# Optimization experiments

Measured on AMD Instinct MI355X. Metric: run time of the kernel, lower is better.

Reference implementation:

```python
import jax, jax.numpy as jnp
import numpy as np

NSMP = 8192
NA = 512  # min_in_features
DOUT = 256  # out_features
REALNA = 520  # input.shape[1] - nSmp


def setup_inputs() -> dict:
    key = jax.random.key(0)
    k1, k2 = jax.random.split(key)
    inp = jax.random.uniform(k1, (NSMP, REALNA + NSMP), dtype=jnp.float32)
    weight = jax.random.uniform(k2, (NA, DOUT), dtype=jnp.float32)  # torch.rand init
    return {"input": inp, "weight": weight}


def reference(input, weight):
    nSmp = NSMP
    na = NA
    X = input[:, :na]  # [nSmp, na]
    realna = input.shape[1] - nSmp
    A = input[:, realna - 8:realna + nSmp - 8]  # [nSmp, nSmp]
    A = A + jnp.eye(nSmp, dtype=input.dtype)
    # D = diag(colsum(A)); D_hat = inverse(D)**0.5 == diag(d^{-1/2})
    d = jnp.sum(A, axis=0)
    d_inv_sqrt = jax.lax.rsqrt(d)
    # DAD = D_hat @ A @ D_hat, applied as row/col scaling (exploits diagonal structure)
    DAD = d_inv_sqrt[:, None] * A * d_inv_sqrt[None, :]
    support = X @ weight  # [nSmp, out]
    output = DAD @ support  # [nSmp, out]
    # bias=False in init, so no bias add
    return jnp.concatenate((output, A), axis=1)  # [nSmp, out + nSmp]
```

## Files before the change

kernel.cpp:

```cpp
#include <hip/hip_runtime.h>

#define NSMP 8192
#define INW  8712
#define OUTW 8448
#define AOFF 512
#define DO   256

typedef __attribute__((ext_vector_type(4)))  float f32x4;
typedef __attribute__((ext_vector_type(8)))  short short8;
typedef __attribute__((ext_vector_type(16))) float floatx16;

typedef __attribute__((address_space(1))) const unsigned int* gptr_t;
typedef __attribute__((address_space(3)))       unsigned int* lptr_t;

__device__ __forceinline__ unsigned pk_bf16(float lo, float hi) {
    return (__float_as_uint(lo) >> 16) | (__float_as_uint(hi) & 0xffff0000u);
}

__device__ __forceinline__ void gload_lds16(const void* g, void* l) {
    __builtin_amdgcn_global_load_lds((gptr_t)g, (lptr_t)l, 16, 0, 0);
}

__global__ __launch_bounds__(256) void kcopy(const float* __restrict__ in,
                                             float* __restrict__ out,
                                             float* __restrict__ d) {
    const int t  = threadIdx.x;
    const int j0 = blockIdx.x * 1024;
    const int i0 = blockIdx.y * 32;
    const int jc = j0 + 4 * t;
    const float* src = in  + (size_t)i0 * INW  + AOFF + jc;
    float*       dst = out + (size_t)i0 * OUTW + DO   + jc;
    f32x4 cs = {0.f, 0.f, 0.f, 0.f};
#pragma unroll 8
    for (int r = 0; r < 32; ++r) {
        f32x4 v = *(const f32x4*)(src + (size_t)r * INW);
        int di = (i0 + r) - j0;
        if ((di >> 2) == t) {
            int s = di & 3;
            v[0] += (s == 0); v[1] += (s == 1); v[2] += (s == 2); v[3] += (s == 3);
        }
        cs += v;
        __builtin_nontemporal_store(v, (f32x4*)(dst + (size_t)r * OUTW));
    }
    atomicAdd(&d[jc + 0], cs[0]);
    atomicAdd(&d[jc + 1], cs[1]);
    atomicAdd(&d[jc + 2], cs[2]);
    atomicAdd(&d[jc + 3], cs[3]);
}

__global__ __launch_bounds__(256) void ksupport(const float* __restrict__ in,
                                                const float* __restrict__ w,
                                                const float* __restrict__ d,
                                                float* __restrict__ dinv,
                                                unsigned short* __restrict__ sP) {
    const int c  = threadIdx.x;
    const int r0 = blockIdx.x * 8;
    const float* X = in + (size_t)r0 * INW;
    float acc[8] = {0.f, 0.f, 0.f, 0.f, 0.f, 0.f, 0.f, 0.f};
#pragma unroll 4
    for (int k = 0; k < 512; ++k) {
        float wv = w[(size_t)k * DO + c];
#pragma unroll
        for (int r = 0; r < 8; ++r)
            acc[r] = fmaf(X[(size_t)r * INW + k], wv, acc[r]);
    }
    union { unsigned short h[8]; uint4 u; } pk;
#pragma unroll
    for (int r = 0; r < 8; ++r) {
        float dv = rsqrtf(d[r0 + r]);
        unsigned ub = __float_as_uint(acc[r] * dv);
        ub += 0x7fffu + ((ub >> 16) & 1u);
        pk.h[r] = (unsigned short)(ub >> 16);
    }
    *(uint4*)(sP + (size_t)(r0 >> 3) * (DO * 8) + (size_t)c * 8) = pk.u;
    if (c < 8) dinv[r0 + c] = rsqrtf(d[r0 + c]);
}

__global__ __launch_bounds__(256, 2) void kmm(const float* __restrict__ in,
                                              const unsigned short* __restrict__ sP,
                                              const float* __restrict__ dinv,
                                              float* __restrict__ out) {
    __shared__ __align__(16) float          lA[2][32 * 64];
    __shared__ __align__(16) unsigned short lB[2][8 * 128 * 8];

    const int b  = blockIdx.x;
    const int rg = ((b >> 4) << 3) + (b & 7);
    const int ch = (b >> 3) & 1;
    const int tid = threadIdx.x;
    const int w = tid >> 6, lane = tid & 63;
    const int m = lane & 31, q = lane >> 5;
    const int i0 = rg * 32;
    const int cc = ch * 128 + w * 32 + m;

    const int subr = lane >> 4;
    const int gl   = lane & 15;
    const int lrA0 = w * 8;

    floatx16 acc;
#pragma unroll
    for (int z = 0; z < 16; ++z) acc[z] = 0.f;

    auto stage = [&](int nb, int s) {
        const int k0 = s * 64;
#pragma unroll
        for (int t = 0; t < 2; ++t) {
            const int lr = lrA0 + t * 4 + subr;
            const float* g = in + (size_t)(i0 + lr) * INW + AOFF + k0 + 4 * (gl ^ (lr & 7));
            gload_lds16(g, &lA[nb][(lrA0 + t * 4) * 64]);
        }
#pragma unroll
        for (int j = 0; j < 4; ++j) {
            const int oct  = 2 * w + (j >> 1);
            const int ch64 = j & 1;
            const unsigned short* g = sP + (size_t)(s * 8 + oct) * (DO * 8)
                                        + (size_t)(ch * 128 + ch64 * 64 + lane) * 8;
            gload_lds16(g, &lB[nb][(oct * 128 + ch64 * 64) * 8]);
        }
    };

    stage(0, 0);
    __syncthreads();

    for (int s = 0; s < 128; ++s) {
        const int cur = s & 1;
        if (s + 1 < 128) stage(cur ^ 1, s + 1);
        const float*          lAc = lA[cur];
        const unsigned short* lBc = lB[cur];
#pragma unroll
        for (int ks = 0; ks < 4; ++ks) {
            const int gbase = ks * 4 + q * 2;
            const int g0 = gbase ^ (m & 7);
            const int g1 = (gbase + 1) ^ (m & 7);
            f32x4 a0 = *(const f32x4*)(lAc + m * 64 + g0 * 4);
            f32x4 a1 = *(const f32x4*)(lAc + m * 64 + g1 * 4);
            uint4 bq = *(const uint4*)(lBc + ((size_t)(2 * ks + q) * 128 + w * 32 + m) * 8);
            union { unsigned u[4]; short8 s8; } fa;
            fa.u[0] = pk_bf16(a0[0], a0[1]); fa.u[1] = pk_bf16(a0[2], a0[3]);
            fa.u[2] = pk_bf16(a1[0], a1[1]); fa.u[3] = pk_bf16(a1[2], a1[3]);
            union { uint4 q4; short8 s8; } fb; fb.q4 = bq;
            acc = __builtin_amdgcn_mfma_f32_32x32x16_bf16(fa.s8, fb.s8, acc, 0, 0, 0);
        }
        __syncthreads();
    }

#pragma unroll
    for (int g = 0; g < 4; ++g) {
        const ushort4 s4 = *(const ushort4*)(sP + (size_t)(i0 / 8 + g) * (DO * 8)
                                                + (size_t)cc * 8 + 4 * q);
        unsigned short sv[4] = {s4.x, s4.y, s4.z, s4.w};
#pragma unroll
        for (int rr = 0; rr < 4; ++rr) {
            const int row = i0 + 8 * g + 4 * q + rr;
            const float idt = __uint_as_float(((unsigned)sv[rr]) << 16);
            out[(size_t)row * OUTW + cc] = (acc[g * 4 + rr] + idt) * dinv[row];
        }
    }
}

extern "C" void kernel_launch(void* const* d_in, const int* in_sizes, int n_in,
                              void* d_out, int out_size, void* d_ws, size_t ws_size,
                              hipStream_t stream) {
    (void)in_sizes; (void)n_in; (void)out_size; (void)ws_size;
    const float* in = (const float*)d_in[0];
    const float* w  = (const float*)d_in[1];
    float* out  = (float*)d_out;
    float* d    = (float*)d_ws;
    float* dinv = d + NSMP;
    unsigned short* sP = (unsigned short*)(d + 2 * NSMP);

    hipMemsetAsync(d, 0, NSMP * sizeof(float), stream);
    kcopy<<<dim3(8, 256), 256, 0, stream>>>(in, out, d);
    ksupport<<<1024, 256, 0, stream>>>(in, w, d, dinv, sP);
    kmm<<<512, 256, 0, stream>>>(in, sP, dinv, out);
}
```

Measured before the change: 671.4 us.

## Emit bf16 copy of A in copy kernel and stream it in matmul

The copy kernel now also writes a bf16 version of A (without the identity) into workspace, so the matmul kernel reads half the bytes for A and skips the per-iteration fp32-to-bf16 packing. The B operand (scaled support) is now loaded straight into registers instead of through shared memory, and the main loop is unrolled by two with explicit double buffering. This adds an extra 128MB bf16 write in the copy kernel in exchange for reading 128MB instead of 256MB in the matmul. A-loads in the copy kernel are also marked nontemporal.

```diff
diff --git a/kernel.cpp b/kernel.cpp
--- a/kernel.cpp
+++ b/kernel.cpp
@@ -23,17 +23,23 @@
 
 __global__ __launch_bounds__(256) void kcopy(const float* __restrict__ in,
                                              float* __restrict__ out,
-                                             float* __restrict__ d) {
+                                             float* __restrict__ d,
+                                             unsigned short* __restrict__ aP) {
     const int t  = threadIdx.x;
     const int j0 = blockIdx.x * 1024;
     const int i0 = blockIdx.y * 32;
     const int jc = j0 + 4 * t;
-    const float* src = in  + (size_t)i0 * INW  + AOFF + jc;
-    float*       dst = out + (size_t)i0 * OUTW + DO   + jc;
+    const float*    src = in  + (size_t)i0 * INW  + AOFF + jc;
+    float*          dst = out + (size_t)i0 * OUTW + DO   + jc;
+    unsigned short* ap  = aP  + (size_t)i0 * NSMP + jc;
     f32x4 cs = {0.f, 0.f, 0.f, 0.f};
 #pragma unroll 8
     for (int r = 0; r < 32; ++r) {
-        f32x4 v = *(const f32x4*)(src + (size_t)r * INW);
+        f32x4 v = __builtin_nontemporal_load((const f32x4*)(src + (size_t)r * INW));
+        uint2 pb;
+        pb.x = pk_bf16(v[0], v[1]);
+        pb.y = pk_bf16(v[2], v[3]);
+        *(uint2*)(ap + (size_t)r * NSMP) = pb;
         int di = (i0 + r) - j0;
         if ((di >> 2) == t) {
             int s = di & 3;
@@ -76,12 +82,11 @@
     if (c < 8) dinv[r0 + c] = rsqrtf(d[r0 + c]);
 }
 
-__global__ __launch_bounds__(256, 2) void kmm(const float* __restrict__ in,
+__global__ __launch_bounds__(256, 2) void kmm(const unsigned short* __restrict__ aP,
                                               const unsigned short* __restrict__ sP,
                                               const float* __restrict__ dinv,
                                               float* __restrict__ out) {
-    __shared__ __align__(16) float          lA[2][32 * 64];
-    __shared__ __align__(16) unsigned short lB[2][8 * 128 * 8];
+    __shared__ __align__(16) unsigned short lA[2][32 * 64];
 
     const int b  = blockIdx.x;
     const int rg = ((b >> 4) << 3) + (b & 7);
@@ -92,56 +97,56 @@
     const int i0 = rg * 32;
     const int cc = ch * 128 + w * 32 + m;
 
-    const int subr = lane >> 4;
-    const int gl   = lane & 15;
-    const int lrA0 = w * 8;
+    const int srow = lane >> 3;
+    const int sg   = lane & 7;
+    const unsigned short* aSrc = aP + (size_t)(i0 + w * 8 + srow) * NSMP
+                                    + 8 * (sg ^ (srow & 7));
+    const unsigned short* bB   = sP + (size_t)q * 2048 + (size_t)cc * 8;
 
     floatx16 acc;
 #pragma unroll
     for (int z = 0; z < 16; ++z) acc[z] = 0.f;
 
-    auto stage = [&](int nb, int s) {
-        const int k0 = s * 64;
-#pragma unroll
-        for (int t = 0; t < 2; ++t) {
-            const int lr = lrA0 + t * 4 + subr;
-            const float* g = in + (size_t)(i0 + lr) * INW + AOFF + k0 + 4 * (gl ^ (lr & 7));
-            gload_lds16(g, &lA[nb][(lrA0 + t * 4) * 64]);
-        }
-#pragma unroll
-        for (int j = 0; j < 4; ++j) {
-            const int oct  = 2 * w + (j >> 1);
-            const int ch64 = j & 1;
-            const unsigned short* g = sP + (size_t)(s * 8 + oct) * (DO * 8)
-                                        + (size_t)(ch * 128 + ch64 * 64 + lane) * 8;
-            gload_lds16(g, &lB[nb][(oct * 128 + ch64 * 64) * 8]);
-        }
-    };
+    uint4 Ba0, Ba1, Ba2, Ba3, Bb0, Bb1, Bb2, Bb3;
 
-    stage(0, 0);
+#define STAGE_A(nb, s) gload_lds16(aSrc + (size_t)(s) * 64, &lA[nb][w * 512])
+#define LOAD_B(P, s) do {                                              \
+        P##0 = *(const uint4*)(bB + (size_t)((s) * 8 + 0) * 2048);     \
+        P##1 = *(const uint4*)(bB + (size_t)((s) * 8 + 2) * 2048);     \
+        P##2 = *(const uint4*)(bB + (size_t)((s) * 8 + 4) * 2048);     \
+        P##3 = *(const uint4*)(bB + (size_t)((s) * 8 + 6) * 2048);     \
+    } while (0)
+#define MFMA_KS(cur, Breg, ks) do {                                    \
+        union { uint4 u; short8 s8; } fb_; fb_.u = Breg;               \
+        const short8 af_ = *(const short8*)(                           \
+            &lA[cur][m * 64 + ((((ks) * 2 + q) ^ (m & 7)) * 8)]);      \
+        acc = __builtin_amdgcn_mfma_f32_32x32x16_bf16(af_, fb_.s8, acc, 0, 0, 0); \
+    } while (0)
+#define COMPUTE(cur, P) do {                                           \
+        MFMA_KS(cur, P##0, 0); MFMA_KS(cur, P##1, 1);                  \
+        MFMA_KS(cur, P##2, 2); MFMA_KS(cur, P##3, 3);                  \
+    } while (0)
+
+    STAGE_A(0, 0);
+    LOAD_B(Ba, 0);
     __syncthreads();
 
-    for (int s = 0; s < 128; ++s) {
-        const int cur = s & 1;
-        if (s + 1 < 128) stage(cur ^ 1, s + 1);
-        const float*          lAc = lA[cur];
-        const unsigned short* lBc = lB[cur];
-#pragma unroll
-        for (int ks = 0; ks < 4; ++ks) {
-            const int gbase = ks * 4 + q * 2;
-            const int g0 = gbase ^ (m & 7);
-            const int g1 = (gbase + 1) ^ (m & 7);
-            f32x4 a0 = *(const f32x4*)(lAc + m * 64 + g0 * 4);
-            f32x4 a1 = *(const f32x4*)(lAc + m * 64 + g1 * 4);
-            uint4 bq = *(const uint4*)(lBc + ((size_t)(2 * ks + q) * 128 + w * 32 + m) * 8);
-            union { unsigned u[4]; short8 s8; } fa;
-            fa.u[0] = pk_bf16(a0[0], a0[1]); fa.u[1] = pk_bf16(a0[2], a0[3]);
-            fa.u[2] = pk_bf16(a1[0], a1[1]); fa.u[3] = pk_bf16(a1[2], a1[3]);
-            union { uint4 q4; short8 s8; } fb; fb.q4 = bq;
-            acc = __builtin_amdgcn_mfma_f32_32x32x16_bf16(fa.s8, fb.s8, acc, 0, 0, 0);
-        }
+    for (int s = 0; s < 128; s += 2) {
+        STAGE_A(1, s + 1);
+        LOAD_B(Bb, s + 1);
+        COMPUTE(0, Ba);
+        __syncthreads();
+        const int s2 = (s + 2 < 128) ? s + 2 : 0;
+        STAGE_A(0, s2);
+        LOAD_B(Ba, s2);
+        COMPUTE(1, Bb);
         __syncthreads();
     }
+
+#undef STAGE_A
+#undef LOAD_B
+#undef MFMA_KS
+#undef COMPUTE
 
 #pragma unroll
     for (int g = 0; g < 4; ++g) {
@@ -167,9 +172,10 @@
     float* d    = (float*)d_ws;
     float* dinv = d + NSMP;
     unsigned short* sP = (unsigned short*)(d + 2 * NSMP);
+    unsigned short* aP = sP + (size_t)1024 * DO * 8;
 
     hipMemsetAsync(d, 0, NSMP * sizeof(float), stream);
-    kcopy<<<dim3(8, 256), 256, 0, stream>>>(in, out, d);
+    kcopy<<<dim3(8, 256), 256, 0, stream>>>(in, out, d, aP);
     ksupport<<<1024, 256, 0, stream>>>(in, w, d, dinv, sP);
-    kmm<<<512, 256, 0, stream>>>(in, sP, dinv, out);
+    kmm<<<512, 256, 0, stream>>>(aP, sP, dinv, out);
 }
```

New measurement: 624.1 us. 7.0% less time.
